# Performance work log

Hardware: AMD Instinct MI355X
Metric: run time of the kernel (lower is better)

The kernel has to match this reference:

```python
import jax, jax.numpy as jnp
import numpy as np

IN_C, HID, LSTM_H, OUT_C = 128, 128, 128, 2
N_NODES, N_EDGES, N_GRAPHS = 100000, 1600000, 256


def gcn_conv(x, src, dst, W, b, n_nodes):
    # h = XW, then symmetric-normalized aggregation with self loops (PyG GCNConv defaults)
    h = x @ W  # [N, H]
    loop = jnp.arange(n_nodes)
    s = jnp.concatenate([src, loop])
    d = jnp.concatenate([dst, loop])
    deg = jax.ops.segment_sum(jnp.ones_like(d, dtype=h.dtype), d, num_segments=n_nodes)
    dinv = jnp.where(deg > 0, jax.lax.rsqrt(deg), 0.0)
    norm = dinv[s] * dinv[d]  # [E+N]
    out = jax.ops.segment_sum(norm[:, None] * h[s], d, num_segments=n_nodes)
    return out + b


def setup_inputs() -> dict:
    key = jax.random.key(0)
    ks = jax.random.split(key, 16)
    x = jax.random.normal(ks[0], (N_NODES, IN_C), dtype=jnp.float32)
    edge_index = jax.random.randint(ks[1], (2, N_EDGES), 0, N_NODES)
    batch = jnp.sort(jax.random.randint(ks[2], (N_NODES,), 0, N_GRAPHS))
    sc = lambda *shape: 1.0 / np.sqrt(shape[0])
    W0 = jax.random.normal(ks[3], (IN_C, HID), jnp.float32) * sc(IN_C)
    b0 = jnp.zeros((HID,), jnp.float32)
    W1 = jax.random.normal(ks[4], (HID, HID), jnp.float32) * sc(HID)
    b1 = jnp.zeros((HID,), jnp.float32)
    W2 = jax.random.normal(ks[5], (HID, HID), jnp.float32) * sc(HID)
    b2 = jnp.zeros((HID,), jnp.float32)
    W_ih = jax.random.normal(ks[6], (4 * LSTM_H, HID), jnp.float32) * sc(HID)
    W_hh = jax.random.normal(ks[7], (4 * LSTM_H, LSTM_H), jnp.float32) * sc(LSTM_H)
    b_ih = jnp.zeros((4 * LSTM_H,), jnp.float32)
    b_hh = jnp.zeros((4 * LSTM_H,), jnp.float32)
    W_fc = jax.random.normal(ks[8], (OUT_C, LSTM_H), jnp.float32) * sc(LSTM_H)
    b_fc = jnp.zeros((OUT_C,), jnp.float32)
    return dict(x=x, edge_index=edge_index, batch=batch, num_graphs=N_GRAPHS,
                W0=W0, b0=b0, W1=W1, b1=b1, W2=W2, b2=b2,
                W_ih=W_ih, W_hh=W_hh, b_ih=b_ih, b_hh=b_hh, W_fc=W_fc, b_fc=b_fc)


def reference(x, edge_index, batch, num_graphs, W0, b0, W1, b1, W2, b2,
              W_ih, W_hh, b_ih, b_hh, W_fc, b_fc):
    n_nodes = x.shape[0]
    src, dst = edge_index[0], edge_index[1]
    h = x
    for W, b in ((W0, b0), (W1, b1), (W2, b2)):
        h = jax.nn.relu(gcn_conv(h, src, dst, W, b, n_nodes))
    # dropout: identity in eval mode
    # global_mean_pool over batch ids
    sums = jax.ops.segment_sum(h, batch, num_segments=num_graphs)  # [G, HID]
    cnts = jax.ops.segment_sum(jnp.ones((n_nodes,), h.dtype), batch, num_segments=num_graphs)
    pooled = sums / jnp.maximum(cnts, 1.0)[:, None]
    # single-step LSTM from zero state: h0 = c0 = 0 => W_hh contributes 0
    g = pooled @ W_ih.T + b_ih + b_hh  # [G, 4H]
    i, f, gg, o = jnp.split(g, 4, axis=-1)  # PyTorch gate order i,f,g,o
    c = jax.nn.sigmoid(i) * jnp.tanh(gg)
    hn = jax.nn.sigmoid(o) * jnp.tanh(c)
    return hn @ W_fc.T + b_fc
```

## Files before the change

kernel.cpp:

```cpp
#include <hip/hip_runtime.h>
#include <math.h>
#include <stdint.h>

#define HID 128
#define SCAN_CHUNK 1024
#define NBUCK_MAX 512
#define EDGE_TILE 8192
#define GEMM_ROWS 128
#define XS_STRIDE 136

typedef short bf16x8 __attribute__((ext_vector_type(8)));
typedef float f32x4 __attribute__((ext_vector_type(4)));

__device__ __forceinline__ unsigned int f2bf(float f) {
    union { float f; uint32_t i; } u; u.f = f;
    uint32_t r = u.i + 0x7fffu + ((u.i >> 16) & 1u);
    return r >> 16;
}

__global__ __launch_bounds__(256) void scan_phase1(const int* __restrict__ cnt,
                                                   int* __restrict__ blockSums,
                                                   float* __restrict__ dinv, int nN) {
    __shared__ int sdata[256];
    const int t = threadIdx.x;
    const int idx = blockIdx.x * SCAN_CHUNK + t * 4;
    int v0 = 0, v1 = 0, v2 = 0, v3 = 0;
    if (idx + 3 < nN) {
        int4 v = *(const int4*)(cnt + idx);
        v0 = v.x; v1 = v.y; v2 = v.z; v3 = v.w;
        float4 dv;
        dv.x = rsqrtf((float)v0 + 1.0f);
        dv.y = rsqrtf((float)v1 + 1.0f);
        dv.z = rsqrtf((float)v2 + 1.0f);
        dv.w = rsqrtf((float)v3 + 1.0f);
        *(float4*)(dinv + idx) = dv;
    } else {
        if (idx     < nN) { v0 = cnt[idx];     dinv[idx]     = rsqrtf((float)v0 + 1.0f); }
        if (idx + 1 < nN) { v1 = cnt[idx + 1]; dinv[idx + 1] = rsqrtf((float)v1 + 1.0f); }
        if (idx + 2 < nN) { v2 = cnt[idx + 2]; dinv[idx + 2] = rsqrtf((float)v2 + 1.0f); }
        if (idx + 3 < nN) { v3 = cnt[idx + 3]; dinv[idx + 3] = rsqrtf((float)v3 + 1.0f); }
    }
    sdata[t] = v0 + v1 + v2 + v3;
    __syncthreads();
#pragma unroll
    for (int off = 128; off > 0; off >>= 1) {
        if (t < off) sdata[t] += sdata[t + off];
        __syncthreads();
    }
    if (t == 0) blockSums[blockIdx.x] = sdata[0];
}

__global__ __launch_bounds__(256) void scan_phase2(int* __restrict__ blockSums, int nB) {
    __shared__ int sd[256];
    const int t = threadIdx.x;
    sd[t] = (t < nB) ? blockSums[t] : 0;
    __syncthreads();
#pragma unroll
    for (int off = 1; off < 256; off <<= 1) {
        int v = sd[t];
        int add = (t >= off) ? sd[t - off] : 0;
        __syncthreads();
        sd[t] = v + add;
        __syncthreads();
    }
    if (t < nB) blockSums[t] = (t > 0) ? sd[t - 1] : 0;
}

__global__ __launch_bounds__(256) void scan_phase3(const int* __restrict__ cnt,
                                                   const int* __restrict__ blockOffsets,
                                                   int* __restrict__ rowptr, int nN, int nE) {
    __shared__ int sdata[256];
    const int t = threadIdx.x;
    const int idx = blockIdx.x * SCAN_CHUNK + t * 4;
    int v0 = 0, v1 = 0, v2 = 0, v3 = 0;
    if (idx + 3 < nN) {
        int4 v = *(const int4*)(cnt + idx);
        v0 = v.x; v1 = v.y; v2 = v.z; v3 = v.w;
    } else {
        if (idx     < nN) v0 = cnt[idx];
        if (idx + 1 < nN) v1 = cnt[idx + 1];
        if (idx + 2 < nN) v2 = cnt[idx + 2];
        if (idx + 3 < nN) v3 = cnt[idx + 3];
    }
    sdata[t] = v0 + v1 + v2 + v3;
    __syncthreads();
#pragma unroll
    for (int off = 1; off < 256; off <<= 1) {
        int v = sdata[t];
        int add = (t >= off) ? sdata[t - off] : 0;
        __syncthreads();
        sdata[t] = v + add;
        __syncthreads();
    }
    const int pre = blockOffsets[blockIdx.x] + ((t > 0) ? sdata[t - 1] : 0);
    if (idx + 3 < nN) {
        *(int4*)(rowptr + idx) = make_int4(pre, pre + v0, pre + v0 + v1, pre + v0 + v1 + v2);
    } else {
        if (idx     < nN) rowptr[idx]     = pre;
        if (idx + 1 < nN) rowptr[idx + 1] = pre + v0;
        if (idx + 2 < nN) rowptr[idx + 2] = pre + v0 + v1;
        if (idx + 3 < nN) rowptr[idx + 3] = pre + v0 + v1 + v2;
    }
    if (blockIdx.x == 0 && t == 0) rowptr[nN] = nE;
}

__global__ __launch_bounds__(256) void bucket_count(const int* __restrict__ dst,
                                                    int* __restrict__ bcnt, int nE, int nB) {
    __shared__ int h[NBUCK_MAX];
    for (int i = threadIdx.x; i < nB; i += 256) h[i] = 0;
    __syncthreads();
    const int base = blockIdx.x * EDGE_TILE;
    const int end = min(base + EDGE_TILE, nE);
    for (int e = base + threadIdx.x; e < end; e += 256)
        atomicAdd(&h[dst[e] >> 8], 1);
    __syncthreads();
    for (int i = threadIdx.x; i < nB; i += 256)
        if (h[i]) atomicAdd(&bcnt[i], h[i]);
}

__global__ __launch_bounds__(512) void bucket_scan(const int* __restrict__ bcnt,
                                                   int* __restrict__ boff,
                                                   int* __restrict__ bcur, int nB) {
    __shared__ int sd[512];
    const int t = threadIdx.x;
    sd[t] = (t < nB) ? bcnt[t] : 0;
    __syncthreads();
#pragma unroll
    for (int off = 1; off < 512; off <<= 1) {
        int v = sd[t];
        int add = (t >= off) ? sd[t - off] : 0;
        __syncthreads();
        sd[t] = v + add;
        __syncthreads();
    }
    if (t < nB) {
        int ex = (t > 0) ? sd[t - 1] : 0;
        boff[t] = ex;
        bcur[t] = ex;
    }
}

__global__ __launch_bounds__(256) void bucket_scatter(const int* __restrict__ src,
                                                      const int* __restrict__ dst,
                                                      int* __restrict__ bcur,
                                                      unsigned int* __restrict__ ebuf,
                                                      int nE, int nB) {
    __shared__ int h[NBUCK_MAX];
    __shared__ int basearr[NBUCK_MAX];
    const int base = blockIdx.x * EDGE_TILE;
    const int end = min(base + EDGE_TILE, nE);
    for (int i = threadIdx.x; i < nB; i += 256) h[i] = 0;
    __syncthreads();
    for (int e = base + threadIdx.x; e < end; e += 256)
        atomicAdd(&h[dst[e] >> 8], 1);
    __syncthreads();
    for (int i = threadIdx.x; i < nB; i += 256) {
        int c = h[i];
        basearr[i] = c ? atomicAdd(&bcur[i], c) : 0;
        h[i] = 0;
    }
    __syncthreads();
    for (int e = base + threadIdx.x; e < end; e += 256) {
        int d = dst[e];
        int b = d >> 8;
        int pos = basearr[b] + atomicAdd(&h[b], 1);
        ebuf[pos] = ((unsigned)src[e] << 8) | ((unsigned)d & 255u);
    }
}

__global__ __launch_bounds__(256) void node_count(const unsigned int* __restrict__ ebuf,
                                                  const int* __restrict__ boff,
                                                  int* __restrict__ cnt, int nE, int nB, int nN) {
    __shared__ int h[256];
    h[threadIdx.x] = 0;
    __syncthreads();
    const int b = blockIdx.x;
    const int e0 = boff[b];
    const int e1 = (b + 1 < nB) ? boff[b + 1] : nE;
    for (int e = e0 + threadIdx.x; e < e1; e += 256)
        atomicAdd(&h[ebuf[e] & 255u], 1);
    __syncthreads();
    const int v = b * 256 + threadIdx.x;
    if (v < nN) cnt[v] = h[threadIdx.x];
}

__global__ __launch_bounds__(256) void csr_from_buckets(const unsigned int* __restrict__ ebuf,
                                                        const int* __restrict__ boff,
                                                        const int* __restrict__ rowptr,
                                                        int* __restrict__ ssrc, int nE, int nB) {
    __shared__ int cur[256];
    const int b = blockIdx.x;
    const int e0 = boff[b];
    const int e1 = (b + 1 < nB) ? boff[b + 1] : nE;
    const int nodeBase = b * 256;
    cur[threadIdx.x] = 0;
    __syncthreads();
    for (int e = e0 + threadIdx.x; e < e1; e += 256) {
        unsigned int ed = ebuf[e];
        int li = (int)(ed & 255u);
        int pos = rowptr[nodeBase + li] + atomicAdd(&cur[li], 1);
        ssrc[pos] = (int)(ed >> 8);
    }
}

__global__ __launch_bounds__(256) void wt_kernel(const float* __restrict__ W0,
                                                 const float* __restrict__ W1,
                                                 const float* __restrict__ W2,
                                                 unsigned short* __restrict__ Wtb) {
    int i = blockIdx.x * 256 + threadIdx.x;
    if (i < 3 * HID * HID) {
        int w = i >> 14, r = i & 16383;
        int n = r >> 7, k = r & 127;
        const float* W = (w == 0) ? W0 : (w == 1) ? W1 : W2;
        Wtb[i] = (unsigned short)f2bf(W[k * HID + n]);
    }
}

__global__ __launch_bounds__(256) void gemm_mfma_f32in(const float* __restrict__ X,
                                                       const uint4* __restrict__ Wtb,
                                                       const float* __restrict__ dinv,
                                                       unsigned int* __restrict__ Pb32,
                                                       int nN) {
    __shared__ short Xs[GEMM_ROWS * XS_STRIDE];
    __shared__ short Ws[HID * XS_STRIDE];
    const int tid = threadIdx.x;
    const int rowBase = blockIdx.x * GEMM_ROWS;
#pragma unroll
    for (int it = 0; it < 16; ++it) {
        int f = it * 256 + tid;
        int row = f >> 5, c = f & 31;
        int grow = rowBase + row;
        float4 v = make_float4(0.f, 0.f, 0.f, 0.f);
        if (grow < nN) v = *(const float4*)(X + (size_t)grow * HID + c * 4);
        uint2 o;
        o.x = f2bf(v.x) | (f2bf(v.y) << 16);
        o.y = f2bf(v.z) | (f2bf(v.w) << 16);
        *(uint2*)(&Xs[row * XS_STRIDE + c * 4]) = o;
    }
#pragma unroll
    for (int it = 0; it < 8; ++it) {
        int f = it * 256 + tid;
        int n = f >> 4, c = f & 15;
        *(uint4*)(&Ws[n * XS_STRIDE + c * 8]) = Wtb[f];
    }
    __syncthreads();
    const int wave = tid >> 6, lane = tid & 63;
    const int quad = lane >> 4, l16 = lane & 15;
    f32x4 acc[2][8] = {};
    const int kq = quad * 8;
#pragma unroll
    for (int ks = 0; ks < 4; ++ks) {
        const int k0 = ks * 32 + kq;
        bf16x8 a0 = *(const bf16x8*)(&Xs[(wave * 32 + l16) * XS_STRIDE + k0]);
        bf16x8 a1 = *(const bf16x8*)(&Xs[(wave * 32 + 16 + l16) * XS_STRIDE + k0]);
#pragma unroll
        for (int nt = 0; nt < 8; ++nt) {
            bf16x8 b = *(const bf16x8*)(&Ws[(nt * 16 + l16) * XS_STRIDE + k0]);
            acc[0][nt] = __builtin_amdgcn_mfma_f32_16x16x32_bf16(a0, b, acc[0][nt], 0, 0, 0);
            acc[1][nt] = __builtin_amdgcn_mfma_f32_16x16x32_bf16(a1, b, acc[1][nt], 0, 0, 0);
        }
    }
#pragma unroll
    for (int mt = 0; mt < 2; ++mt) {
        const int gr0 = rowBase + wave * 32 + mt * 16 + quad * 4;
#pragma unroll
        for (int r = 0; r < 4; ++r) {
            const int gr = gr0 + r;
            const bool ok = gr < nN;
            const float d = ok ? dinv[gr] : 0.f;
#pragma unroll
            for (int nt = 0; nt < 8; ++nt) {
                float v = d * acc[mt][nt][r];
                float vo = __shfl_xor(v, 1, 64);
                if (ok && !(l16 & 1)) {
                    Pb32[(size_t)gr * 64 + nt * 8 + (l16 >> 1)] = f2bf(v) | (f2bf(vo) << 16);
                }
            }
        }
    }
}

__device__ __forceinline__ void acc_bf8(const uint4 q, float* a) {
    union { uint32_t i; float f; } t;
    t.i = q.x << 16;          a[0] += t.f;
    t.i = q.x & 0xffff0000u;  a[1] += t.f;
    t.i = q.y << 16;          a[2] += t.f;
    t.i = q.y & 0xffff0000u;  a[3] += t.f;
    t.i = q.z << 16;          a[4] += t.f;
    t.i = q.z & 0xffff0000u;  a[5] += t.f;
    t.i = q.w << 16;          a[6] += t.f;
    t.i = q.w & 0xffff0000u;  a[7] += t.f;
}

__global__ __launch_bounds__(256) void fused_agg_gemm(const uint4* __restrict__ Pb,
                                                      const int* __restrict__ rowptr,
                                                      const int* __restrict__ ssrc,
                                                      const float* __restrict__ dinv,
                                                      const float* __restrict__ bias,
                                                      const unsigned short* __restrict__ Wtb,
                                                      unsigned int* __restrict__ Pout32,
                                                      int nN) {
    __shared__ short Hs[16 * XS_STRIDE];
    const int tid = threadIdx.x;
    const int lane16 = tid & 15;
    const int grp = tid >> 4;
    const int v = blockIdx.x * 16 + grp;
    const bool ok = v < nN;
    float a0[8], a1[8], a2[8], a3[8];
#pragma unroll
    for (int i = 0; i < 8; ++i) { a0[i] = 0.f; a1[i] = 0.f; a2[i] = 0.f; a3[i] = 0.f; }
    uint4 q = make_uint4(0u, 0u, 0u, 0u);
    if (ok) {
        acc_bf8(Pb[(size_t)v * 16 + lane16], a0);
        int e = rowptr[v];
        const int e1 = rowptr[v + 1];
        for (; e + 4 <= e1; e += 4) {
            const int u0 = ssrc[e + 0], u1 = ssrc[e + 1], u2 = ssrc[e + 2], u3 = ssrc[e + 3];
            uint4 q0 = Pb[(size_t)u0 * 16 + lane16];
            uint4 q1 = Pb[(size_t)u1 * 16 + lane16];
            uint4 q2 = Pb[(size_t)u2 * 16 + lane16];
            uint4 q3 = Pb[(size_t)u3 * 16 + lane16];
            acc_bf8(q0, a0); acc_bf8(q1, a1); acc_bf8(q2, a2); acc_bf8(q3, a3);
        }
        for (; e < e1; ++e) {
            uint4 qe = Pb[(size_t)ssrc[e] * 16 + lane16];
            acc_bf8(qe, a1);
        }
        const float dv = dinv[v];
        const float4 bb0 = ((const float4*)bias)[lane16 * 2];
        const float4 bb1 = ((const float4*)bias)[lane16 * 2 + 1];
        float4 o0, o1;
        o0.x = fmaxf(fmaf(dv, (a0[0] + a1[0]) + (a2[0] + a3[0]), bb0.x), 0.f);
        o0.y = fmaxf(fmaf(dv, (a0[1] + a1[1]) + (a2[1] + a3[1]), bb0.y), 0.f);
        o0.z = fmaxf(fmaf(dv, (a0[2] + a1[2]) + (a2[2] + a3[2]), bb0.z), 0.f);
        o0.w = fmaxf(fmaf(dv, (a0[3] + a1[3]) + (a2[3] + a3[3]), bb0.w), 0.f);
        o1.x = fmaxf(fmaf(dv, (a0[4] + a1[4]) + (a2[4] + a3[4]), bb1.x), 0.f);
        o1.y = fmaxf(fmaf(dv, (a0[5] + a1[5]) + (a2[5] + a3[5]), bb1.y), 0.f);
        o1.z = fmaxf(fmaf(dv, (a0[6] + a1[6]) + (a2[6] + a3[6]), bb1.z), 0.f);
        o1.w = fmaxf(fmaf(dv, (a0[7] + a1[7]) + (a2[7] + a3[7]), bb1.w), 0.f);
        q.x = f2bf(o0.x) | (f2bf(o0.y) << 16);
        q.y = f2bf(o0.z) | (f2bf(o0.w) << 16);
        q.z = f2bf(o1.x) | (f2bf(o1.y) << 16);
        q.w = f2bf(o1.z) | (f2bf(o1.w) << 16);
    }
    *(uint4*)(&Hs[grp * XS_STRIDE + lane16 * 8]) = q;
    __syncthreads();
    const int wave = tid >> 6, lane = tid & 63;
    const int quad = lane >> 4, l16 = lane & 15;
    f32x4 acc[2] = {};
#pragma unroll
    for (int ks = 0; ks < 4; ++ks) {
        const int k0 = ks * 32 + quad * 8;
        bf16x8 a = *(const bf16x8*)(&Hs[l16 * XS_STRIDE + k0]);
#pragma unroll
        for (int nt = 0; nt < 2; ++nt) {
            const int n = (wave * 2 + nt) * 16 + l16;
            bf16x8 b = *(const bf16x8*)((const short*)Wtb + (size_t)n * HID + k0);
            acc[nt] = __builtin_amdgcn_mfma_f32_16x16x32_bf16(a, b, acc[nt], 0, 0, 0);
        }
    }
#pragma unroll
    for (int r = 0; r < 4; ++r) {
        const int gr = blockIdx.x * 16 + quad * 4 + r;
        const bool okr = gr < nN;
        const float d = okr ? dinv[gr] : 0.f;
#pragma unroll
        for (int nt = 0; nt < 2; ++nt) {
            float val = d * acc[nt][r];
            float vo = __shfl_xor(val, 1, 64);
            if (okr && !(l16 & 1)) {
                Pout32[(size_t)gr * 64 + (wave * 2 + nt) * 8 + (l16 >> 1)] =
                    f2bf(val) | (f2bf(vo) << 16);
            }
        }
    }
}

__global__ __launch_bounds__(256) void agg_pool_kernel(const uint4* __restrict__ Pb,
                                                       const int* __restrict__ rowptr,
                                                       const int* __restrict__ ssrc,
                                                       const float* __restrict__ dinv,
                                                       const float* __restrict__ bias,
                                                       const int* __restrict__ batch,
                                                       float* __restrict__ psum, int nN) {
    __shared__ float Hf[16][HID + 1];
    __shared__ int bg[16];
    const int tid = threadIdx.x;
    const int lane = tid & 15;
    const int grp = tid >> 4;
    const int v = blockIdx.x * 16 + grp;
    const bool ok = v < nN;
    float a0[8], a1[8], a2[8], a3[8];
#pragma unroll
    for (int i = 0; i < 8; ++i) { a0[i] = 0.f; a1[i] = 0.f; a2[i] = 0.f; a3[i] = 0.f; }
    float4 o0 = make_float4(0.f, 0.f, 0.f, 0.f), o1 = o0;
    if (ok) {
        acc_bf8(Pb[(size_t)v * 16 + lane], a0);
        int e = rowptr[v];
        const int e1 = rowptr[v + 1];
        for (; e + 4 <= e1; e += 4) {
            const int u0 = ssrc[e + 0], u1 = ssrc[e + 1], u2 = ssrc[e + 2], u3 = ssrc[e + 3];
            uint4 q0 = Pb[(size_t)u0 * 16 + lane];
            uint4 q1 = Pb[(size_t)u1 * 16 + lane];
            uint4 q2 = Pb[(size_t)u2 * 16 + lane];
            uint4 q3 = Pb[(size_t)u3 * 16 + lane];
            acc_bf8(q0, a0); acc_bf8(q1, a1); acc_bf8(q2, a2); acc_bf8(q3, a3);
        }
        for (; e < e1; ++e) {
            uint4 q = Pb[(size_t)ssrc[e] * 16 + lane];
            acc_bf8(q, a1);
        }
        const float dv = dinv[v];
        const float4 bb0 = ((const float4*)bias)[lane * 2];
        const float4 bb1 = ((const float4*)bias)[lane * 2 + 1];
        o0.x = fmaxf(fmaf(dv, (a0[0] + a1[0]) + (a2[0] + a3[0]), bb0.x), 0.f);
        o0.y = fmaxf(fmaf(dv, (a0[1] + a1[1]) + (a2[1] + a3[1]), bb0.y), 0.f);
        o0.z = fmaxf(fmaf(dv, (a0[2] + a1[2]) + (a2[2] + a3[2]), bb0.z), 0.f);
        o0.w = fmaxf(fmaf(dv, (a0[3] + a1[3]) + (a2[3] + a3[3]), bb0.w), 0.f);
        o1.x = fmaxf(fmaf(dv, (a0[4] + a1[4]) + (a2[4] + a3[4]), bb1.x), 0.f);
        o1.y = fmaxf(fmaf(dv, (a0[5] + a1[5]) + (a2[5] + a3[5]), bb1.y), 0.f);
        o1.z = fmaxf(fmaf(dv, (a0[6] + a1[6]) + (a2[6] + a3[6]), bb1.z), 0.f);
        o1.w = fmaxf(fmaf(dv, (a0[7] + a1[7]) + (a2[7] + a3[7]), bb1.w), 0.f);
    }
    *(float4*)(&Hf[grp][lane * 8]) = o0;
    *(float4*)(&Hf[grp][lane * 8 + 4]) = o1;
    if (lane == 0) bg[grp] = ok ? batch[v] : -1;
    __syncthreads();
    if (tid < HID) {
        const int c = tid;
        float acc = 0.f;
        int g = -1;
#pragma unroll
        for (int i = 0; i < 16; ++i) {
            const int gi = bg[i];
            if (gi < 0) continue;
            const float val = Hf[i][c];
            if (gi != g) {
                if (g >= 0) atomicAdd(&psum[g * HID + c], acc);
                g = gi;
                acc = val;
            } else {
                acc += val;
            }
        }
        if (g >= 0) atomicAdd(&psum[g * HID + c], acc);
    }
}

__global__ __launch_bounds__(128) void pool_finalize(const float* __restrict__ psum,
                                                     const int* __restrict__ batch,
                                                     float* __restrict__ pooled, int nN) {
    const int g = blockIdx.x;
    int lo = 0, hi = nN;
    while (lo < hi) { int m = (lo + hi) >> 1; if (batch[m] < g) lo = m + 1; else hi = m; }
    const int start = lo;
    hi = nN;
    while (lo < hi) { int m = (lo + hi) >> 1; if (batch[m] < g + 1) lo = m + 1; else hi = m; }
    const float c = (float)max(lo - start, 1);
    pooled[g * HID + threadIdx.x] = psum[g * HID + threadIdx.x] / c;
}

__device__ __forceinline__ float sigmoidf_(float x) { return 1.0f / (1.0f + expf(-x)); }

__global__ __launch_bounds__(128) void lstm_fc_kernel(const float* __restrict__ pooled,
                                                      const float* __restrict__ W_ih,
                                                      const float* __restrict__ b_ih,
                                                      const float* __restrict__ b_hh,
                                                      const float* __restrict__ W_fc,
                                                      const float* __restrict__ b_fc,
                                                      float* __restrict__ out) {
    __shared__ float pv[HID];
    __shared__ float r0[2], r1[2];
    const int g = blockIdx.x, j = threadIdx.x;
    pv[j] = pooled[g * HID + j];
    __syncthreads();
    float di = b_ih[j] + b_hh[j];
    float dg = b_ih[256 + j] + b_hh[256 + j];
    float dO = b_ih[384 + j] + b_hh[384 + j];
    const float4* pv4 = (const float4*)pv;
#pragma unroll 4
    for (int k4 = 0; k4 < 32; ++k4) {
        float4 p = pv4[k4];
        float4 wi = *(const float4*)(W_ih + (size_t)j * HID + k4 * 4);
        float4 wg = *(const float4*)(W_ih + (size_t)(256 + j) * HID + k4 * 4);
        float4 wo = *(const float4*)(W_ih + (size_t)(384 + j) * HID + k4 * 4);
        di += p.x * wi.x + p.y * wi.y + p.z * wi.z + p.w * wi.w;
        dg += p.x * wg.x + p.y * wg.y + p.z * wg.z + p.w * wg.w;
        dO += p.x * wo.x + p.y * wo.y + p.z * wo.z + p.w * wo.w;
    }
    float c = sigmoidf_(di) * tanhf(dg);
    float hn = sigmoidf_(dO) * tanhf(c);
    float p0 = hn * W_fc[j];
    float p1 = hn * W_fc[HID + j];
#pragma unroll
    for (int off = 32; off > 0; off >>= 1) {
        p0 += __shfl_down(p0, off, 64);
        p1 += __shfl_down(p1, off, 64);
    }
    const int w = j >> 6, l = j & 63;
    if (l == 0) { r0[w] = p0; r1[w] = p1; }
    __syncthreads();
    if (j == 0) {
        out[g * 2 + 0] = r0[0] + r0[1] + b_fc[0];
        out[g * 2 + 1] = r1[0] + r1[1] + b_fc[1];
    }
}

extern "C" void kernel_launch(void* const* d_in, const int* in_sizes, int n_in,
                              void* d_out, int out_size, void* d_ws, size_t ws_size,
                              hipStream_t stream) {
    const float* x      = (const float*)d_in[0];
    const int*   eidx   = (const int*)d_in[1];
    const int*   batch  = (const int*)d_in[2];
    const float* W0     = (const float*)d_in[4];
    const float* b0     = (const float*)d_in[5];
    const float* W1     = (const float*)d_in[6];
    const float* b1     = (const float*)d_in[7];
    const float* W2     = (const float*)d_in[8];
    const float* b2     = (const float*)d_in[9];
    const float* W_ih   = (const float*)d_in[10];
    const float* b_ih   = (const float*)d_in[12];
    const float* b_hh   = (const float*)d_in[13];
    const float* W_fc   = (const float*)d_in[14];
    const float* b_fc   = (const float*)d_in[15];
    float* out = (float*)d_out;

    const int nN = in_sizes[0] / HID;
    const int nE = in_sizes[1] / 2;
    const int nG = out_size / 2;
    const int* src = eidx;
    const int* dst = eidx + nE;
    const int rowsPad = (nN + GEMM_ROWS - 1) & ~(GEMM_ROWS - 1);

    size_t off = 0;
    auto alloc = [&](size_t bytes) -> void* {
        void* p = (char*)d_ws + off;
        off += (bytes + 255) & ~(size_t)255;
        return p;
    };
    uint4* Pb     = (uint4*)alloc((size_t)nN * 16 * sizeof(uint4));
    uint4* Pb2    = (uint4*)alloc((size_t)nN * 16 * sizeof(uint4));
    float* dinv   = (float*)alloc((size_t)nN * sizeof(float));
    int*   cnt    = (int*)alloc((size_t)nN * sizeof(int));
    int*   rowptr = (int*)alloc((size_t)(nN + 1) * sizeof(int));
    int*   ssrc   = (int*)alloc((size_t)nE * sizeof(int));
    unsigned int* ebuf = (unsigned int*)alloc((size_t)nE * sizeof(unsigned int));
    float* pooled = (float*)alloc((size_t)nG * HID * sizeof(float));
    float* psum   = (float*)alloc((size_t)nG * HID * sizeof(float));
    int*   blockSums = (int*)alloc(1024 * sizeof(int));
    int*   bcnt   = (int*)alloc(NBUCK_MAX * sizeof(int));
    int*   boff   = (int*)alloc(NBUCK_MAX * sizeof(int));
    int*   bcur   = (int*)alloc(NBUCK_MAX * sizeof(int));
    unsigned short* Wtb = (unsigned short*)alloc(3 * HID * HID * sizeof(unsigned short));
    (void)ws_size;

    const int scanBlocks = (nN + SCAN_CHUNK - 1) / SCAN_CHUNK;
    const int nB = (nN + 255) >> 8;
    const int tileBlocks = (nE + EDGE_TILE - 1) / EDGE_TILE;

    hipMemsetAsync(bcnt, 0, NBUCK_MAX * sizeof(int), stream);
    bucket_count<<<tileBlocks, 256, 0, stream>>>(dst, bcnt, nE, nB);
    bucket_scan<<<1, 512, 0, stream>>>(bcnt, boff, bcur, nB);
    bucket_scatter<<<tileBlocks, 256, 0, stream>>>(src, dst, bcur, ebuf, nE, nB);

    node_count<<<nB, 256, 0, stream>>>(ebuf, boff, cnt, nE, nB, nN);
    scan_phase1<<<scanBlocks, 256, 0, stream>>>(cnt, blockSums, dinv, nN);
    scan_phase2<<<1, 256, 0, stream>>>(blockSums, scanBlocks);
    scan_phase3<<<scanBlocks, 256, 0, stream>>>(cnt, blockSums, rowptr, nN, nE);
    csr_from_buckets<<<nB, 256, 0, stream>>>(ebuf, boff, rowptr, ssrc, nE, nB);

    wt_kernel<<<(3 * HID * HID + 255) / 256, 256, 0, stream>>>(W0, W1, W2, Wtb);

    const int gemmBlocks = rowsPad / GEMM_ROWS;
    const int aggBlocks = (nN + 15) / 16;
    const unsigned short* Wt1 = Wtb + HID * HID;
    const unsigned short* Wt2 = Wtb + 2 * HID * HID;

    hipMemsetAsync(psum, 0, (size_t)nG * HID * sizeof(float), stream);

    gemm_mfma_f32in<<<gemmBlocks, 256, 0, stream>>>(x, (const uint4*)Wtb, dinv,
                                                    (unsigned int*)Pb, nN);
    fused_agg_gemm<<<aggBlocks, 256, 0, stream>>>(Pb, rowptr, ssrc, dinv, b0, Wt1,
                                                  (unsigned int*)Pb2, nN);
    fused_agg_gemm<<<aggBlocks, 256, 0, stream>>>(Pb2, rowptr, ssrc, dinv, b1, Wt2,
                                                  (unsigned int*)Pb, nN);
    agg_pool_kernel<<<aggBlocks, 256, 0, stream>>>(Pb, rowptr, ssrc, dinv, b2,
                                                   batch, psum, nN);

    pool_finalize<<<nG, 128, 0, stream>>>(psum, batch, pooled, nN);
    lstm_fc_kernel<<<nG, 128, 0, stream>>>(pooled, W_ih, b_ih, b_hh, W_fc, b_fc, out);
}
```

Measured before the change: 466.7 us.

## Renumber nodes by (graph, degree) to balance aggregation and keep pooling contiguous

Adds a counting sort of nodes keyed by graph id and clamped in-degree, building perm/inv arrays. The CSR, dinv, batch ids and GEMM input rows are all built in the permuted order, and source indices are remapped through inv. The aim is that each aggregation block handles nodes of similar degree, which reduces wavefront imbalance, while pooling still sees graph-contiguous rows. The cost is extra preprocessing kernels plus indirect gathers of x rows and of cnt.

```diff
diff --git a/kernel.cpp b/kernel.cpp
--- a/kernel.cpp
+++ b/kernel.cpp
@@ -8,6 +8,7 @@
 #define EDGE_TILE 8192
 #define GEMM_ROWS 128
 #define XS_STRIDE 136
+#define DEG_BINS 64
 
 typedef short bf16x8 __attribute__((ext_vector_type(8)));
 typedef float f32x4 __attribute__((ext_vector_type(4)));
@@ -16,92 +17,6 @@
     union { float f; uint32_t i; } u; u.f = f;
     uint32_t r = u.i + 0x7fffu + ((u.i >> 16) & 1u);
     return r >> 16;
-}
-
-__global__ __launch_bounds__(256) void scan_phase1(const int* __restrict__ cnt,
-                                                   int* __restrict__ blockSums,
-                                                   float* __restrict__ dinv, int nN) {
-    __shared__ int sdata[256];
-    const int t = threadIdx.x;
-    const int idx = blockIdx.x * SCAN_CHUNK + t * 4;
-    int v0 = 0, v1 = 0, v2 = 0, v3 = 0;
-    if (idx + 3 < nN) {
-        int4 v = *(const int4*)(cnt + idx);
-        v0 = v.x; v1 = v.y; v2 = v.z; v3 = v.w;
-        float4 dv;
-        dv.x = rsqrtf((float)v0 + 1.0f);
-        dv.y = rsqrtf((float)v1 + 1.0f);
-        dv.z = rsqrtf((float)v2 + 1.0f);
-        dv.w = rsqrtf((float)v3 + 1.0f);
-        *(float4*)(dinv + idx) = dv;
-    } else {
-        if (idx     < nN) { v0 = cnt[idx];     dinv[idx]     = rsqrtf((float)v0 + 1.0f); }
-        if (idx + 1 < nN) { v1 = cnt[idx + 1]; dinv[idx + 1] = rsqrtf((float)v1 + 1.0f); }
-        if (idx + 2 < nN) { v2 = cnt[idx + 2]; dinv[idx + 2] = rsqrtf((float)v2 + 1.0f); }
-        if (idx + 3 < nN) { v3 = cnt[idx + 3]; dinv[idx + 3] = rsqrtf((float)v3 + 1.0f); }
-    }
-    sdata[t] = v0 + v1 + v2 + v3;
-    __syncthreads();
-#pragma unroll
-    for (int off = 128; off > 0; off >>= 1) {
-        if (t < off) sdata[t] += sdata[t + off];
-        __syncthreads();
-    }
-    if (t == 0) blockSums[blockIdx.x] = sdata[0];
-}
-
-__global__ __launch_bounds__(256) void scan_phase2(int* __restrict__ blockSums, int nB) {
-    __shared__ int sd[256];
-    const int t = threadIdx.x;
-    sd[t] = (t < nB) ? blockSums[t] : 0;
-    __syncthreads();
-#pragma unroll
-    for (int off = 1; off < 256; off <<= 1) {
-        int v = sd[t];
-        int add = (t >= off) ? sd[t - off] : 0;
-        __syncthreads();
-        sd[t] = v + add;
-        __syncthreads();
-    }
-    if (t < nB) blockSums[t] = (t > 0) ? sd[t - 1] : 0;
-}
-
-__global__ __launch_bounds__(256) void scan_phase3(const int* __restrict__ cnt,
-                                                   const int* __restrict__ blockOffsets,
-                                                   int* __restrict__ rowptr, int nN, int nE) {
-    __shared__ int sdata[256];
-    const int t = threadIdx.x;
-    const int idx = blockIdx.x * SCAN_CHUNK + t * 4;
-    int v0 = 0, v1 = 0, v2 = 0, v3 = 0;
-    if (idx + 3 < nN) {
-        int4 v = *(const int4*)(cnt + idx);
-        v0 = v.x; v1 = v.y; v2 = v.z; v3 = v.w;
-    } else {
-        if (idx     < nN) v0 = cnt[idx];
-        if (idx + 1 < nN) v1 = cnt[idx + 1];
-        if (idx + 2 < nN) v2 = cnt[idx + 2];
-        if (idx + 3 < nN) v3 = cnt[idx + 3];
-    }
-    sdata[t] = v0 + v1 + v2 + v3;
-    __syncthreads();
-#pragma unroll
-    for (int off = 1; off < 256; off <<= 1) {
-        int v = sdata[t];
-        int add = (t >= off) ? sdata[t - off] : 0;
-        __syncthreads();
-        sdata[t] = v + add;
-        __syncthreads();
-    }
-    const int pre = blockOffsets[blockIdx.x] + ((t > 0) ? sdata[t - 1] : 0);
-    if (idx + 3 < nN) {
-        *(int4*)(rowptr + idx) = make_int4(pre, pre + v0, pre + v0 + v1, pre + v0 + v1 + v2);
-    } else {
-        if (idx     < nN) rowptr[idx]     = pre;
-        if (idx + 1 < nN) rowptr[idx + 1] = pre + v0;
-        if (idx + 2 < nN) rowptr[idx + 2] = pre + v0 + v1;
-        if (idx + 3 < nN) rowptr[idx + 3] = pre + v0 + v1 + v2;
-    }
-    if (blockIdx.x == 0 && t == 0) rowptr[nN] = nE;
 }
 
 __global__ __launch_bounds__(256) void bucket_count(const int* __restrict__ dst,
@@ -184,22 +99,163 @@
     if (v < nN) cnt[v] = h[threadIdx.x];
 }
 
+__global__ __launch_bounds__(256) void key_hist(const int* __restrict__ batch,
+                                                const int* __restrict__ cnt,
+                                                int* __restrict__ bins, int nN) {
+    int v = blockIdx.x * 256 + threadIdx.x;
+    if (v < nN) {
+        int k = batch[v] * DEG_BINS + min(cnt[v], DEG_BINS - 1);
+        atomicAdd(&bins[k], 1);
+    }
+}
+
+__global__ __launch_bounds__(1024) void key_scan(int* __restrict__ bins,
+                                                 int* __restrict__ binCur, int nBins) {
+    __shared__ int sums[1024];
+    const int t = threadIdx.x;
+    const int base = t * 16;
+    int vals[16];
+    int local = 0;
+#pragma unroll
+    for (int j = 0; j < 16; ++j) {
+        vals[j] = (base + j < nBins) ? bins[base + j] : 0;
+        local += vals[j];
+    }
+    sums[t] = local;
+    __syncthreads();
+#pragma unroll
+    for (int off = 1; off < 1024; off <<= 1) {
+        int v = sums[t];
+        int add = (t >= off) ? sums[t - off] : 0;
+        __syncthreads();
+        sums[t] = v + add;
+        __syncthreads();
+    }
+    int run = (t > 0) ? sums[t - 1] : 0;
+#pragma unroll
+    for (int j = 0; j < 16; ++j) {
+        if (base + j < nBins) {
+            int c = vals[j];
+            bins[base + j] = run;
+            binCur[base + j] = run;
+            run += c;
+        }
+    }
+}
+
+__global__ __launch_bounds__(256) void key_scatter(const int* __restrict__ batch,
+                                                   const int* __restrict__ cnt,
+                                                   int* __restrict__ binCur,
+                                                   int* __restrict__ perm,
+                                                   int* __restrict__ inv, int nN) {
+    int v = blockIdx.x * 256 + threadIdx.x;
+    if (v < nN) {
+        int k = batch[v] * DEG_BINS + min(cnt[v], DEG_BINS - 1);
+        int idx = atomicAdd(&binCur[k], 1);
+        perm[idx] = v;
+        inv[v] = idx;
+    }
+}
+
+__global__ __launch_bounds__(256) void scan_phase1(const int* __restrict__ cnt,
+                                                   const int* __restrict__ perm,
+                                                   const int* __restrict__ batch,
+                                                   int* __restrict__ blockSums,
+                                                   float* __restrict__ dinv,
+                                                   int* __restrict__ bnew, int nN) {
+    __shared__ int sdata[256];
+    const int t = threadIdx.x;
+    const int idx = blockIdx.x * SCAN_CHUNK + t * 4;
+    int total = 0;
+#pragma unroll
+    for (int j = 0; j < 4; ++j) {
+        int i = idx + j;
+        if (i < nN) {
+            int p = perm[i];
+            int c = cnt[p];
+            dinv[i] = rsqrtf((float)c + 1.0f);
+            bnew[i] = batch[p];
+            total += c;
+        }
+    }
+    sdata[t] = total;
+    __syncthreads();
+#pragma unroll
+    for (int off = 128; off > 0; off >>= 1) {
+        if (t < off) sdata[t] += sdata[t + off];
+        __syncthreads();
+    }
+    if (t == 0) blockSums[blockIdx.x] = sdata[0];
+}
+
+__global__ __launch_bounds__(256) void scan_phase2(int* __restrict__ blockSums, int nB) {
+    __shared__ int sd[256];
+    const int t = threadIdx.x;
+    sd[t] = (t < nB) ? blockSums[t] : 0;
+    __syncthreads();
+#pragma unroll
+    for (int off = 1; off < 256; off <<= 1) {
+        int v = sd[t];
+        int add = (t >= off) ? sd[t - off] : 0;
+        __syncthreads();
+        sd[t] = v + add;
+        __syncthreads();
+    }
+    if (t < nB) blockSums[t] = (t > 0) ? sd[t - 1] : 0;
+}
+
+__global__ __launch_bounds__(256) void scan_phase3(const int* __restrict__ cnt,
+                                                   const int* __restrict__ perm,
+                                                   const int* __restrict__ blockOffsets,
+                                                   int* __restrict__ rowptr, int nN, int nE) {
+    __shared__ int sdata[256];
+    const int t = threadIdx.x;
+    const int idx = blockIdx.x * SCAN_CHUNK + t * 4;
+    int v0 = 0, v1 = 0, v2 = 0, v3 = 0;
+    if (idx     < nN) v0 = cnt[perm[idx]];
+    if (idx + 1 < nN) v1 = cnt[perm[idx + 1]];
+    if (idx + 2 < nN) v2 = cnt[perm[idx + 2]];
+    if (idx + 3 < nN) v3 = cnt[perm[idx + 3]];
+    sdata[t] = v0 + v1 + v2 + v3;
+    __syncthreads();
+#pragma unroll
+    for (int off = 1; off < 256; off <<= 1) {
+        int v = sdata[t];
+        int add = (t >= off) ? sdata[t - off] : 0;
+        __syncthreads();
+        sdata[t] = v + add;
+        __syncthreads();
+    }
+    const int pre = blockOffsets[blockIdx.x] + ((t > 0) ? sdata[t - 1] : 0);
+    if (idx     < nN) rowptr[idx]     = pre;
+    if (idx + 1 < nN) rowptr[idx + 1] = pre + v0;
+    if (idx + 2 < nN) rowptr[idx + 2] = pre + v0 + v1;
+    if (idx + 3 < nN) rowptr[idx + 3] = pre + v0 + v1 + v2;
+    if (blockIdx.x == 0 && t == 0) rowptr[nN] = nE;
+}
+
 __global__ __launch_bounds__(256) void csr_from_buckets(const unsigned int* __restrict__ ebuf,
                                                         const int* __restrict__ boff,
                                                         const int* __restrict__ rowptr,
-                                                        int* __restrict__ ssrc, int nE, int nB) {
+                                                        const int* __restrict__ inv,
+                                                        int* __restrict__ ssrc,
+                                                        int nE, int nB, int nN) {
     __shared__ int cur[256];
+    __shared__ int rp[256];
+    const int t = threadIdx.x;
     const int b = blockIdx.x;
     const int e0 = boff[b];
     const int e1 = (b + 1 < nB) ? boff[b + 1] : nE;
     const int nodeBase = b * 256;
-    cur[threadIdx.x] = 0;
-    __syncthreads();
-    for (int e = e0 + threadIdx.x; e < e1; e += 256) {
+    cur[t] = 0;
+    const int vOld = nodeBase + t;
+    rp[t] = (vOld < nN) ? rowptr[inv[vOld]] : 0;
+    __syncthreads();
+    for (int e = e0 + t; e < e1; e += 256) {
         unsigned int ed = ebuf[e];
         int li = (int)(ed & 255u);
-        int pos = rowptr[nodeBase + li] + atomicAdd(&cur[li], 1);
-        ssrc[pos] = (int)(ed >> 8);
+        int pos = rp[li] + atomicAdd(&cur[li], 1);
+        ssrc[pos] = inv[ed >> 8];
     }
 }
 
@@ -217,6 +273,7 @@
 }
 
 __global__ __launch_bounds__(256) void gemm_mfma_f32in(const float* __restrict__ X,
+                                                       const int* __restrict__ perm,
                                                        const uint4* __restrict__ Wtb,
                                                        const float* __restrict__ dinv,
                                                        unsigned int* __restrict__ Pb32,
@@ -231,7 +288,10 @@
         int row = f >> 5, c = f & 31;
         int grow = rowBase + row;
         float4 v = make_float4(0.f, 0.f, 0.f, 0.f);
-        if (grow < nN) v = *(const float4*)(X + (size_t)grow * HID + c * 4);
+        if (grow < nN) {
+            int po = perm[grow];
+            v = *(const float4*)(X + (size_t)po * HID + c * 4);
+        }
         uint2 o;
         o.x = f2bf(v.x) | (f2bf(v.y) << 16);
         o.y = f2bf(v.z) | (f2bf(v.w) << 16);
@@ -381,7 +441,7 @@
                                                        const int* __restrict__ ssrc,
                                                        const float* __restrict__ dinv,
                                                        const float* __restrict__ bias,
-                                                       const int* __restrict__ batch,
+                                                       const int* __restrict__ bnew,
                                                        float* __restrict__ psum, int nN) {
     __shared__ float Hf[16][HID + 1];
     __shared__ int bg[16];
@@ -424,7 +484,7 @@
     }
     *(float4*)(&Hf[grp][lane * 8]) = o0;
     *(float4*)(&Hf[grp][lane * 8 + 4]) = o1;
-    if (lane == 0) bg[grp] = ok ? batch[v] : -1;
+    if (lane == 0) bg[grp] = ok ? bnew[v] : -1;
     __syncthreads();
     if (tid < HID) {
         const int c = tid;
@@ -531,6 +591,7 @@
     const int* src = eidx;
     const int* dst = eidx + nE;
     const int rowsPad = (nN + GEMM_ROWS - 1) & ~(GEMM_ROWS - 1);
+    const int nBins = nG * DEG_BINS;
 
     size_t off = 0;
     auto alloc = [&](size_t bytes) -> void* {
@@ -545,6 +606,11 @@
     int*   rowptr = (int*)alloc((size_t)(nN + 1) * sizeof(int));
     int*   ssrc   = (int*)alloc((size_t)nE * sizeof(int));
     unsigned int* ebuf = (unsigned int*)alloc((size_t)nE * sizeof(unsigned int));
+    int*   perm   = (int*)alloc((size_t)nN * sizeof(int));
+    int*   inv    = (int*)alloc((size_t)nN * sizeof(int));
+    int*   bnew   = (int*)alloc((size_t)nN * sizeof(int));
+    int*   bins   = (int*)alloc((size_t)nBins * sizeof(int));
+    int*   binCur = (int*)alloc((size_t)nBins * sizeof(int));
     float* pooled = (float*)alloc((size_t)nG * HID * sizeof(float));
     float* psum   = (float*)alloc((size_t)nG * HID * sizeof(float));
     int*   blockSums = (int*)alloc(1024 * sizeof(int));
@@ -557,17 +623,23 @@
     const int scanBlocks = (nN + SCAN_CHUNK - 1) / SCAN_CHUNK;
     const int nB = (nN + 255) >> 8;
     const int tileBlocks = (nE + EDGE_TILE - 1) / EDGE_TILE;
+    const int nBlocks = (nN + 255) / 256;
 
     hipMemsetAsync(bcnt, 0, NBUCK_MAX * sizeof(int), stream);
+    hipMemsetAsync(bins, 0, (size_t)nBins * sizeof(int), stream);
     bucket_count<<<tileBlocks, 256, 0, stream>>>(dst, bcnt, nE, nB);
     bucket_scan<<<1, 512, 0, stream>>>(bcnt, boff, bcur, nB);
     bucket_scatter<<<tileBlocks, 256, 0, stream>>>(src, dst, bcur, ebuf, nE, nB);
 
     node_count<<<nB, 256, 0, stream>>>(ebuf, boff, cnt, nE, nB, nN);
-    scan_phase1<<<scanBlocks, 256, 0, stream>>>(cnt, blockSums, dinv, nN);
+    key_hist<<<nBlocks, 256, 0, stream>>>(batch, cnt, bins, nN);
+    key_scan<<<1, 1024, 0, stream>>>(bins, binCur, nBins);
+    key_scatter<<<nBlocks, 256, 0, stream>>>(batch, cnt, binCur, perm, inv, nN);
+
+    scan_phase1<<<scanBlocks, 256, 0, stream>>>(cnt, perm, batch, blockSums, dinv, bnew, nN);
     scan_phase2<<<1, 256, 0, stream>>>(blockSums, scanBlocks);
-    scan_phase3<<<scanBlocks, 256, 0, stream>>>(cnt, blockSums, rowptr, nN, nE);
-    csr_from_buckets<<<nB, 256, 0, stream>>>(ebuf, boff, rowptr, ssrc, nE, nB);
+    scan_phase3<<<scanBlocks, 256, 0, stream>>>(cnt, perm, blockSums, rowptr, nN, nE);
+    csr_from_buckets<<<nB, 256, 0, stream>>>(ebuf, boff, rowptr, inv, ssrc, nE, nB, nN);
 
     wt_kernel<<<(3 * HID * HID + 255) / 256, 256, 0, stream>>>(W0, W1, W2, Wtb);
 
@@ -578,14 +650,14 @@
 
     hipMemsetAsync(psum, 0, (size_t)nG * HID * sizeof(float), stream);
 
-    gemm_mfma_f32in<<<gemmBlocks, 256, 0, stream>>>(x, (const uint4*)Wtb, dinv,
+    gemm_mfma_f32in<<<gemmBlocks, 256, 0, stream>>>(x, perm, (const uint4*)Wtb, dinv,
                                                     (unsigned int*)Pb, nN);
     fused_agg_gemm<<<aggBlocks, 256, 0, stream>>>(Pb, rowptr, ssrc, dinv, b0, Wt1,
                                                   (unsigned int*)Pb2, nN);
     fused_agg_gemm<<<aggBlocks, 256, 0, stream>>>(Pb2, rowptr, ssrc, dinv, b1, Wt2,
                                                   (unsigned int*)Pb, nN);
     agg_pool_kernel<<<aggBlocks, 256, 0, stream>>>(Pb, rowptr, ssrc, dinv, b2,
-                                                   batch, psum, nN);
+                                                   bnew, psum, nN);
 
     pool_finalize<<<nG, 128, 0, stream>>>(psum, batch, pooled, nN);
     lstm_fc_kernel<<<nG, 128, 0, stream>>>(pooled, W_ih, b_ih, b_hh, W_fc, b_fc, out);
```

New measurement: 502.8 us. +7.8%, slower.

## Process nodes in degree-sorted order in fused aggregation-GEMM kernels

Applied to the files above, without the earlier changes.

Adds a counting sort of nodes by in-degree (histogram, scan, scatter over 64 bins) and makes fused_agg_gemm process the 16 nodes of each block in that order, so the 16-lane groups in a block see similar edge counts. The aim is to cut load imbalance and idle lanes within blocks during gather-aggregation. It also caches rowptr in shared memory in csr_from_buckets. In exchange it adds three small kernels and an extra order lookup, and consecutive rows in a block are no longer contiguous in memory, so output writes and dinv reads become scattered.

```diff
diff --git a/kernel.cpp b/kernel.cpp
--- a/kernel.cpp
+++ b/kernel.cpp
@@ -8,6 +8,7 @@
 #define EDGE_TILE 8192
 #define GEMM_ROWS 128
 #define XS_STRIDE 136
+#define ORD_BINS 64
 
 typedef short bf16x8 __attribute__((ext_vector_type(8)));
 typedef float f32x4 __attribute__((ext_vector_type(4)));
@@ -16,6 +17,145 @@
     union { float f; uint32_t i; } u; u.f = f;
     uint32_t r = u.i + 0x7fffu + ((u.i >> 16) & 1u);
     return r >> 16;
+}
+
+__global__ __launch_bounds__(256) void bucket_count(const int* __restrict__ dst,
+                                                    int* __restrict__ bcnt, int nE, int nB) {
+    __shared__ int h[NBUCK_MAX];
+    for (int i = threadIdx.x; i < nB; i += 256) h[i] = 0;
+    __syncthreads();
+    const int base = blockIdx.x * EDGE_TILE;
+    const int end = min(base + EDGE_TILE, nE);
+    for (int e = base + threadIdx.x; e < end; e += 256)
+        atomicAdd(&h[dst[e] >> 8], 1);
+    __syncthreads();
+    for (int i = threadIdx.x; i < nB; i += 256)
+        if (h[i]) atomicAdd(&bcnt[i], h[i]);
+}
+
+__global__ __launch_bounds__(512) void bucket_scan(const int* __restrict__ bcnt,
+                                                   int* __restrict__ boff,
+                                                   int* __restrict__ bcur, int nB) {
+    __shared__ int sd[512];
+    const int t = threadIdx.x;
+    sd[t] = (t < nB) ? bcnt[t] : 0;
+    __syncthreads();
+#pragma unroll
+    for (int off = 1; off < 512; off <<= 1) {
+        int v = sd[t];
+        int add = (t >= off) ? sd[t - off] : 0;
+        __syncthreads();
+        sd[t] = v + add;
+        __syncthreads();
+    }
+    if (t < nB) {
+        int ex = (t > 0) ? sd[t - 1] : 0;
+        boff[t] = ex;
+        bcur[t] = ex;
+    }
+}
+
+__global__ __launch_bounds__(256) void bucket_scatter(const int* __restrict__ src,
+                                                      const int* __restrict__ dst,
+                                                      int* __restrict__ bcur,
+                                                      unsigned int* __restrict__ ebuf,
+                                                      int nE, int nB) {
+    __shared__ int h[NBUCK_MAX];
+    __shared__ int basearr[NBUCK_MAX];
+    const int base = blockIdx.x * EDGE_TILE;
+    const int end = min(base + EDGE_TILE, nE);
+    for (int i = threadIdx.x; i < nB; i += 256) h[i] = 0;
+    __syncthreads();
+    for (int e = base + threadIdx.x; e < end; e += 256)
+        atomicAdd(&h[dst[e] >> 8], 1);
+    __syncthreads();
+    for (int i = threadIdx.x; i < nB; i += 256) {
+        int c = h[i];
+        basearr[i] = c ? atomicAdd(&bcur[i], c) : 0;
+        h[i] = 0;
+    }
+    __syncthreads();
+    for (int e = base + threadIdx.x; e < end; e += 256) {
+        int d = dst[e];
+        int b = d >> 8;
+        int pos = basearr[b] + atomicAdd(&h[b], 1);
+        ebuf[pos] = ((unsigned)src[e] << 8) | ((unsigned)d & 255u);
+    }
+}
+
+__global__ __launch_bounds__(256) void node_count(const unsigned int* __restrict__ ebuf,
+                                                  const int* __restrict__ boff,
+                                                  int* __restrict__ cnt, int nE, int nB, int nN) {
+    __shared__ int h[256];
+    h[threadIdx.x] = 0;
+    __syncthreads();
+    const int b = blockIdx.x;
+    const int e0 = boff[b];
+    const int e1 = (b + 1 < nB) ? boff[b + 1] : nE;
+    for (int e = e0 + threadIdx.x; e < e1; e += 256)
+        atomicAdd(&h[ebuf[e] & 255u], 1);
+    __syncthreads();
+    const int v = b * 256 + threadIdx.x;
+    if (v < nN) cnt[v] = h[threadIdx.x];
+}
+
+__global__ __launch_bounds__(256) void dorder_hist(const int* __restrict__ cnt,
+                                                   int* __restrict__ dbins, int nN) {
+    __shared__ int h[ORD_BINS];
+    if (threadIdx.x < ORD_BINS) h[threadIdx.x] = 0;
+    __syncthreads();
+    const int t0 = blockIdx.x * 1024;
+#pragma unroll
+    for (int j = 0; j < 4; ++j) {
+        int i = t0 + threadIdx.x + j * 256;
+        if (i < nN) atomicAdd(&h[min(cnt[i], ORD_BINS - 1)], 1);
+    }
+    __syncthreads();
+    if (threadIdx.x < ORD_BINS && h[threadIdx.x])
+        atomicAdd(&dbins[threadIdx.x], h[threadIdx.x]);
+}
+
+__global__ __launch_bounds__(64) void dorder_scan(int* __restrict__ dbins,
+                                                  int* __restrict__ dcur) {
+    if (threadIdx.x == 0) {
+        int run = 0;
+        for (int i = 0; i < ORD_BINS; ++i) {
+            int c = dbins[i];
+            dbins[i] = run;
+            dcur[i] = run;
+            run += c;
+        }
+    }
+}
+
+__global__ __launch_bounds__(256) void dorder_scatter(const int* __restrict__ cnt,
+                                                      int* __restrict__ dcur,
+                                                      int* __restrict__ order, int nN) {
+    __shared__ int h[ORD_BINS];
+    __shared__ int basearr[ORD_BINS];
+    if (threadIdx.x < ORD_BINS) h[threadIdx.x] = 0;
+    __syncthreads();
+    const int t0 = blockIdx.x * 1024;
+#pragma unroll
+    for (int j = 0; j < 4; ++j) {
+        int i = t0 + threadIdx.x + j * 256;
+        if (i < nN) atomicAdd(&h[min(cnt[i], ORD_BINS - 1)], 1);
+    }
+    __syncthreads();
+    if (threadIdx.x < ORD_BINS) {
+        int c = h[threadIdx.x];
+        basearr[threadIdx.x] = c ? atomicAdd(&dcur[threadIdx.x], c) : 0;
+        h[threadIdx.x] = 0;
+    }
+    __syncthreads();
+#pragma unroll
+    for (int j = 0; j < 4; ++j) {
+        int i = t0 + threadIdx.x + j * 256;
+        if (i < nN) {
+            int b = min(cnt[i], ORD_BINS - 1);
+            order[basearr[b] + atomicAdd(&h[b], 1)] = i;
+        }
+    }
 }
 
 __global__ __launch_bounds__(256) void scan_phase1(const int* __restrict__ cnt,
@@ -104,101 +244,25 @@
     if (blockIdx.x == 0 && t == 0) rowptr[nN] = nE;
 }
 
-__global__ __launch_bounds__(256) void bucket_count(const int* __restrict__ dst,
-                                                    int* __restrict__ bcnt, int nE, int nB) {
-    __shared__ int h[NBUCK_MAX];
-    for (int i = threadIdx.x; i < nB; i += 256) h[i] = 0;
-    __syncthreads();
-    const int base = blockIdx.x * EDGE_TILE;
-    const int end = min(base + EDGE_TILE, nE);
-    for (int e = base + threadIdx.x; e < end; e += 256)
-        atomicAdd(&h[dst[e] >> 8], 1);
-    __syncthreads();
-    for (int i = threadIdx.x; i < nB; i += 256)
-        if (h[i]) atomicAdd(&bcnt[i], h[i]);
-}
-
-__global__ __launch_bounds__(512) void bucket_scan(const int* __restrict__ bcnt,
-                                                   int* __restrict__ boff,
-                                                   int* __restrict__ bcur, int nB) {
-    __shared__ int sd[512];
-    const int t = threadIdx.x;
-    sd[t] = (t < nB) ? bcnt[t] : 0;
-    __syncthreads();
-#pragma unroll
-    for (int off = 1; off < 512; off <<= 1) {
-        int v = sd[t];
-        int add = (t >= off) ? sd[t - off] : 0;
-        __syncthreads();
-        sd[t] = v + add;
-        __syncthreads();
-    }
-    if (t < nB) {
-        int ex = (t > 0) ? sd[t - 1] : 0;
-        boff[t] = ex;
-        bcur[t] = ex;
-    }
-}
-
-__global__ __launch_bounds__(256) void bucket_scatter(const int* __restrict__ src,
-                                                      const int* __restrict__ dst,
-                                                      int* __restrict__ bcur,
-                                                      unsigned int* __restrict__ ebuf,
-                                                      int nE, int nB) {
-    __shared__ int h[NBUCK_MAX];
-    __shared__ int basearr[NBUCK_MAX];
-    const int base = blockIdx.x * EDGE_TILE;
-    const int end = min(base + EDGE_TILE, nE);
-    for (int i = threadIdx.x; i < nB; i += 256) h[i] = 0;
-    __syncthreads();
-    for (int e = base + threadIdx.x; e < end; e += 256)
-        atomicAdd(&h[dst[e] >> 8], 1);
-    __syncthreads();
-    for (int i = threadIdx.x; i < nB; i += 256) {
-        int c = h[i];
-        basearr[i] = c ? atomicAdd(&bcur[i], c) : 0;
-        h[i] = 0;
-    }
-    __syncthreads();
-    for (int e = base + threadIdx.x; e < end; e += 256) {
-        int d = dst[e];
-        int b = d >> 8;
-        int pos = basearr[b] + atomicAdd(&h[b], 1);
-        ebuf[pos] = ((unsigned)src[e] << 8) | ((unsigned)d & 255u);
-    }
-}
-
-__global__ __launch_bounds__(256) void node_count(const unsigned int* __restrict__ ebuf,
-                                                  const int* __restrict__ boff,
-                                                  int* __restrict__ cnt, int nE, int nB, int nN) {
-    __shared__ int h[256];
-    h[threadIdx.x] = 0;
-    __syncthreads();
-    const int b = blockIdx.x;
-    const int e0 = boff[b];
-    const int e1 = (b + 1 < nB) ? boff[b + 1] : nE;
-    for (int e = e0 + threadIdx.x; e < e1; e += 256)
-        atomicAdd(&h[ebuf[e] & 255u], 1);
-    __syncthreads();
-    const int v = b * 256 + threadIdx.x;
-    if (v < nN) cnt[v] = h[threadIdx.x];
-}
-
 __global__ __launch_bounds__(256) void csr_from_buckets(const unsigned int* __restrict__ ebuf,
                                                         const int* __restrict__ boff,
                                                         const int* __restrict__ rowptr,
-                                                        int* __restrict__ ssrc, int nE, int nB) {
+                                                        int* __restrict__ ssrc,
+                                                        int nE, int nB, int nN) {
     __shared__ int cur[256];
+    __shared__ int rp[256];
+    const int t = threadIdx.x;
     const int b = blockIdx.x;
     const int e0 = boff[b];
     const int e1 = (b + 1 < nB) ? boff[b + 1] : nE;
     const int nodeBase = b * 256;
-    cur[threadIdx.x] = 0;
-    __syncthreads();
-    for (int e = e0 + threadIdx.x; e < e1; e += 256) {
+    cur[t] = 0;
+    rp[t] = (nodeBase + t < nN) ? rowptr[nodeBase + t] : 0;
+    __syncthreads();
+    for (int e = e0 + t; e < e1; e += 256) {
         unsigned int ed = ebuf[e];
         int li = (int)(ed & 255u);
-        int pos = rowptr[nodeBase + li] + atomicAdd(&cur[li], 1);
+        int pos = rp[li] + atomicAdd(&cur[li], 1);
         ssrc[pos] = (int)(ed >> 8);
     }
 }
@@ -297,6 +361,7 @@
                                                       const int* __restrict__ ssrc,
                                                       const float* __restrict__ dinv,
                                                       const float* __restrict__ bias,
+                                                      const int* __restrict__ order,
                                                       const unsigned short* __restrict__ Wtb,
                                                       unsigned int* __restrict__ Pout32,
                                                       int nN) {
@@ -304,8 +369,9 @@
     const int tid = threadIdx.x;
     const int lane16 = tid & 15;
     const int grp = tid >> 4;
-    const int v = blockIdx.x * 16 + grp;
-    const bool ok = v < nN;
+    const int oidx = blockIdx.x * 16 + grp;
+    const bool ok = oidx < nN;
+    const int v = ok ? order[oidx] : 0;
     float a0[8], a1[8], a2[8], a3[8];
 #pragma unroll
     for (int i = 0; i < 8; ++i) { a0[i] = 0.f; a1[i] = 0.f; a2[i] = 0.f; a3[i] = 0.f; }
@@ -361,8 +427,9 @@
     }
 #pragma unroll
     for (int r = 0; r < 4; ++r) {
-        const int gr = blockIdx.x * 16 + quad * 4 + r;
-        const bool okr = gr < nN;
+        const int ridx = blockIdx.x * 16 + quad * 4 + r;
+        const bool okr = ridx < nN;
+        const int gr = okr ? order[ridx] : 0;
         const float d = okr ? dinv[gr] : 0.f;
 #pragma unroll
         for (int nt = 0; nt < 2; ++nt) {
@@ -545,6 +612,9 @@
     int*   rowptr = (int*)alloc((size_t)(nN + 1) * sizeof(int));
     int*   ssrc   = (int*)alloc((size_t)nE * sizeof(int));
     unsigned int* ebuf = (unsigned int*)alloc((size_t)nE * sizeof(unsigned int));
+    int*   order  = (int*)alloc((size_t)nN * sizeof(int));
+    int*   dbins  = (int*)alloc(ORD_BINS * sizeof(int));
+    int*   dcur   = (int*)alloc(ORD_BINS * sizeof(int));
     float* pooled = (float*)alloc((size_t)nG * HID * sizeof(float));
     float* psum   = (float*)alloc((size_t)nG * HID * sizeof(float));
     int*   blockSums = (int*)alloc(1024 * sizeof(int));
@@ -557,17 +627,22 @@
     const int scanBlocks = (nN + SCAN_CHUNK - 1) / SCAN_CHUNK;
     const int nB = (nN + 255) >> 8;
     const int tileBlocks = (nE + EDGE_TILE - 1) / EDGE_TILE;
+    const int nodeTiles = (nN + 1023) / 1024;
 
     hipMemsetAsync(bcnt, 0, NBUCK_MAX * sizeof(int), stream);
+    hipMemsetAsync(dbins, 0, ORD_BINS * sizeof(int), stream);
     bucket_count<<<tileBlocks, 256, 0, stream>>>(dst, bcnt, nE, nB);
     bucket_scan<<<1, 512, 0, stream>>>(bcnt, boff, bcur, nB);
     bucket_scatter<<<tileBlocks, 256, 0, stream>>>(src, dst, bcur, ebuf, nE, nB);
 
     node_count<<<nB, 256, 0, stream>>>(ebuf, boff, cnt, nE, nB, nN);
+    dorder_hist<<<nodeTiles, 256, 0, stream>>>(cnt, dbins, nN);
+    dorder_scan<<<1, 64, 0, stream>>>(dbins, dcur);
+    dorder_scatter<<<nodeTiles, 256, 0, stream>>>(cnt, dcur, order, nN);
     scan_phase1<<<scanBlocks, 256, 0, stream>>>(cnt, blockSums, dinv, nN);
     scan_phase2<<<1, 256, 0, stream>>>(blockSums, scanBlocks);
     scan_phase3<<<scanBlocks, 256, 0, stream>>>(cnt, blockSums, rowptr, nN, nE);
-    csr_from_buckets<<<nB, 256, 0, stream>>>(ebuf, boff, rowptr, ssrc, nE, nB);
+    csr_from_buckets<<<nB, 256, 0, stream>>>(ebuf, boff, rowptr, ssrc, nE, nB, nN);
 
     wt_kernel<<<(3 * HID * HID + 255) / 256, 256, 0, stream>>>(W0, W1, W2, Wtb);
 
@@ -580,9 +655,9 @@
 
     gemm_mfma_f32in<<<gemmBlocks, 256, 0, stream>>>(x, (const uint4*)Wtb, dinv,
                                                     (unsigned int*)Pb, nN);
-    fused_agg_gemm<<<aggBlocks, 256, 0, stream>>>(Pb, rowptr, ssrc, dinv, b0, Wt1,
+    fused_agg_gemm<<<aggBlocks, 256, 0, stream>>>(Pb, rowptr, ssrc, dinv, b0, order, Wt1,
                                                   (unsigned int*)Pb2, nN);
-    fused_agg_gemm<<<aggBlocks, 256, 0, stream>>>(Pb2, rowptr, ssrc, dinv, b1, Wt2,
+    fused_agg_gemm<<<aggBlocks, 256, 0, stream>>>(Pb2, rowptr, ssrc, dinv, b1, order, Wt2,
                                                   (unsigned int*)Pb, nN);
     agg_pool_kernel<<<aggBlocks, 256, 0, stream>>>(Pb, rowptr, ssrc, dinv, b2,
                                                    batch, psum, nN);
```

Result: slower. 480.8 us (+3.0%).
